# Kernel optimization log

Hardware: AMD Instinct MI355X
Metric: run time of the kernel (lower is better)

Reference implementation:

```python
import jax, jax.numpy as jnp
import numpy as np

EMBED_DIM = 32
HIDDEN_DIM = 64
N = 1024
LN_EPS = 1e-5


def setup_inputs() -> dict:
    key = jax.random.key(0)
    ks = jax.random.split(key, 8)
    d, h = EMBED_DIM, HIDDEN_DIM
    s1 = 1.0 / np.sqrt(2 * d)
    s2 = 1.0 / np.sqrt(h)
    return {
        "node_embeddings": jax.random.normal(ks[0], (N, d), dtype=jnp.float32),
        # Linear(2d -> h), stored as (2d, h) for x @ W
        "W1": jax.random.uniform(ks[1], (2 * d, h), jnp.float32, -s1, s1),
        "b1": jnp.zeros((h,), jnp.float32),
        "g1": jnp.ones((h,), jnp.float32),
        "be1": jnp.zeros((h,), jnp.float32),
        "W2": jax.random.uniform(ks[2], (h, h), jnp.float32, -s2, s2),
        "b2": jnp.zeros((h,), jnp.float32),
        "g2": jnp.ones((h,), jnp.float32),
        "be2": jnp.zeros((h,), jnp.float32),
        "W3": jax.random.uniform(ks[3], (h, 1), jnp.float32, -s2, s2),
        "b3": jnp.zeros((1,), jnp.float32),
    }


def _layernorm(x, gamma, beta):
    mu = jnp.mean(x, axis=-1, keepdims=True)
    var = jnp.mean(jnp.square(x - mu), axis=-1, keepdims=True)
    return (x - mu) * jax.lax.rsqrt(var + LN_EPS) * gamma + beta


def reference(node_embeddings, W1, b1, g1, be1, W2, b2, g2, be2, W3, b3):
    n, d = node_embeddings.shape
    # pair_emb = cat([src_emb, dst_emb], -1); first linear applied without
    # materializing the concat: split W1 into src/dst halves.
    W1s, W1d = W1[:d], W1[d:]
    hs = node_embeddings @ W1s          # (N, h)
    hd = node_embeddings @ W1d          # (N, h)
    h = hs[:, None, :] + hd[None, :, :] + b1   # (N, N, h)
    h = jax.nn.relu(_layernorm(h, g1, be1))
    h = jax.nn.relu(_layernorm(h @ W2 + b2, g2, be2))
    out = jax.nn.sigmoid((h @ W3 + b3)[..., 0])  # (N, N)
    return out
```

## Files before the change

### kernel.cpp

```cpp
#include <hip/hip_runtime.h>
#include <hip/hip_bf16.h>

#define NN 1024
#define ED 32
#define HD 64
#define LN_EPS 1e-5f

typedef short bf16x8 __attribute__((ext_vector_type(8)));
typedef float f32x4 __attribute__((ext_vector_type(4)));

#define OFF_HS   0
#define OFF_HDB  65536
#define OFF_SS   131072
#define OFF_SD   132096
#define OFF_G1   133120
#define OFF_BE1  133184
#define OFF_B2   133248
#define OFF_G2   133312
#define OFF_BE2  133376
#define OFF_W3   133440
#define OFF_B3   133504
#define OFF_SB2  133505
#define OFF_W2F  133508

__device__ __forceinline__ bool buf_is_f32(const void* g1) {
  return *(const unsigned int*)g1 == 0x3F800000u;
}
template <bool F32>
__device__ __forceinline__ float ld(const void* p, int i) {
  return F32 ? ((const float*)p)[i]
             : __bfloat162float(((const __hip_bfloat16*)p)[i]);
}
__device__ __forceinline__ unsigned short f2bf(float f) {
  unsigned int b = __builtin_bit_cast(unsigned int, f);
  b += 0x7FFFu + ((b >> 16) & 1u);
  return (unsigned short)(b >> 16);
}
__device__ __forceinline__ unsigned int pack2bf(float a, float b) {
  return (unsigned int)f2bf(a) | ((unsigned int)f2bf(b) << 16);
}
__device__ __forceinline__ unsigned int pk_bf(float a, float b) {
  __hip_bfloat162 p = __float22bfloat162_rn(make_float2(a, b));
  unsigned int u;
  __builtin_memcpy(&u, &p, 4);
  return u;
}
__device__ __forceinline__ f32x4 splat4(float v) { f32x4 r = {v, v, v, v}; return r; }

template <int CTRL>
__device__ __forceinline__ float dpp_add(float v) {
  int m = __builtin_amdgcn_update_dpp(0, __builtin_bit_cast(int, v), CTRL, 0xF, 0xF, true);
  return v + __builtin_bit_cast(float, m);
}
template <int CTRL>
__device__ __forceinline__ float dpp_mov(float v) {
  return __builtin_bit_cast(float,
      __builtin_amdgcn_update_dpp(0, __builtin_bit_cast(int, v), CTRL, 0xF, 0xF, true));
}
__device__ __forceinline__ float red16(float v) {
  v = dpp_add<0xB1>(v);
  v = dpp_add<0x4E>(v);
  v = dpp_add<0x124>(v);
  v = dpp_add<0x128>(v);
  return v;
}

template <bool F32>
__device__ void prep_body(const void* E, const void* W1, const void* b1,
                          const void* g1, const void* be1, const void* W2,
                          const void* b2, const void* g2, const void* be2,
                          const void* W3, const void* b3, float* ws) {
  const int i = blockIdx.x, t = threadIdx.x;
  if (i < NN) {
    __shared__ float e[ED];
    if (t < ED) e[t] = ld<F32>(E, i * ED + t);
    __syncthreads();
    int k = t & 63;
    bool dside = t >= 64;
    int wofs = dside ? ED * HD : 0;
    float acc = 0.f;
#pragma unroll
    for (int c = 0; c < ED; ++c)
      acc = fmaf(e[c], ld<F32>(W1, wofs + c * HD + k), acc);
    if (dside) acc += ld<F32>(b1, k);
    float s = acc;
#pragma unroll
    for (int m = 1; m <= 32; m <<= 1) s += __shfl_xor(s, m);
    if (dside) {
      ws[OFF_HDB + i * HD + k] = acc;
      if (k == 0) ws[OFF_SD + i] = s;
    } else {
      ws[OFF_HS + i * HD + k] = acc;
      if (k == 0) ws[OFF_SS + i] = s;
    }
  } else if (i < NN + 16) {
    if (t < 32) {
      int d = (i - NN) * 32 + t;
      int lv = d & 63, nt = (d >> 6) & 3, kc = d >> 8;
      int k0 = kc * 32 + ((lv >> 4) & 3) * 8;
      int n = nt * 16 + (lv & 15);
      unsigned int u4[4];
#pragma unroll
      for (int jj = 0; jj < 4; ++jj)
        u4[jj] = pack2bf(ld<F32>(W2, (k0 + 2 * jj) * HD + n),
                         ld<F32>(W2, (k0 + 2 * jj + 1) * HD + n));
      ((uint4*)(ws + OFF_W2F))[d] = make_uint4(u4[0], u4[1], u4[2], u4[3]);
    }
  } else {
    __shared__ float rs[64];
    if (t < 64) {
      ws[OFF_G1  + t] = ld<F32>(g1,  t);
      ws[OFF_BE1 + t] = ld<F32>(be1, t);
      ws[OFF_B2  + t] = ld<F32>(b2,  t);
      ws[OFF_G2  + t] = ld<F32>(g2,  t);
      ws[OFF_BE2 + t] = ld<F32>(be2, t);
      ws[OFF_W3  + t] = ld<F32>(W3,  t);
      float s = 0.f;
      for (int n = 0; n < HD; ++n) s += ld<F32>(W2, t * HD + n);
      rs[t] = s;
    }
    if (t == 64) {
      float s = 0.f;
      for (int n = 0; n < HD; ++n) s += ld<F32>(b2, n);
      ws[OFF_SB2] = s;
    }
    if (t == 65) ws[OFF_B3] = ld<F32>(b3, 0);
    __syncthreads();
    unsigned short* st = (unsigned short*)(ws + OFF_W2F) + 4096;
    for (int s = t; s < 1024; s += 128) {
      int j = s & 7, lv = (s >> 3) & 63, kc = s >> 9;
      st[s] = f2bf(rs[kc * 32 + ((lv >> 4) & 3) * 8 + j]);
    }
  }
}

__global__ __launch_bounds__(128) void prep_kern(
    const void* E, const void* W1, const void* b1, const void* g1,
    const void* be1, const void* W2, const void* b2, const void* g2,
    const void* be2, const void* W3, const void* b3, float* ws) {
  if (buf_is_f32(g1))
    prep_body<true >(E, W1, b1, g1, be1, W2, b2, g2, be2, W3, b3, ws);
  else
    prep_body<false>(E, W1, b1, g1, be1, W2, b2, g2, be2, W3, b3, ws);
}

__global__ __launch_bounds__(256, 4) void pair_kern(
    const float* __restrict__ ws, float* __restrict__ out) {
  __shared__ float sh[1024];
  __shared__ float sdt[1024];
  __shared__ __align__(16) unsigned int X[256 * 32];
  const int t = threadIdx.x;
  const int bid = blockIdx.x;
  const int lid = (bid & 7) * 512 + (bid >> 3);
  const int bi = lid >> 6, bj = lid & 63;
  const int l = t & 63, w = t >> 6;
  const int q = l >> 4, ln = l & 15;
  const int il = t >> 4, jl = t & 15;
  const float inv = 1.f / 64.f;

  {
    int r = t >> 4, c4 = t & 15;
    ((f32x4*)sh )[r * 16 + (c4 ^ r)] = ((const f32x4*)(ws + OFF_HS  + (bi * 16 + r) * HD))[c4];
    ((f32x4*)sdt)[r * 16 + (c4 ^ r)] = ((const f32x4*)(ws + OFF_HDB + (bj * 16 + r) * HD))[c4];
  }
  const float ssum = ws[OFF_SS + bi * 16 + il];
  const float dsum = ws[OFF_SD + bj * 16 + jl];
  __syncthreads();

  const f32x4* A4 = (const f32x4*)sh;
  const f32x4* B4 = (const f32x4*)sdt;

  float r1, nmu;
  {
    f32x4 q4 = splat4(0.f);
#pragma unroll
    for (int c = 0; c < 16; ++c) {
      f32x4 x = A4[il * 16 + (c ^ il)] + B4[jl * 16 + (c ^ jl)];
      q4 = __builtin_elementwise_fma(x, x, q4);
    }
    float ssq = (q4[0] + q4[1]) + (q4[2] + q4[3]);
    float mu = (ssum + dsum) * inv;
    r1 = rsqrtf(fmaf(-mu, mu, ssq * inv) + LN_EPS);
    nmu = -mu * r1;
  }
  asm volatile("" ::: "memory");

  {
    f32x4 r1v = splat4(r1), nm = splat4(nmu), zero = splat4(0.f);
    uint4* Xr4 = (uint4*)(X + t * 32);
#pragma unroll
    for (int b = 0; b < 8; ++b) {
      unsigned int uu[4];
#pragma unroll
      for (int h = 0; h < 2; ++h) {
        int c = 2 * b + h;
        f32x4 x = A4[il * 16 + (c ^ il)] + B4[jl * 16 + (c ^ jl)];
        f32x4 g, be;
#pragma unroll
        for (int e = 0; e < 4; ++e) {
          g[e]  = ws[OFF_G1  + c * 4 + e];
          be[e] = ws[OFF_BE1 + c * 4 + e];
        }
        f32x4 u = __builtin_elementwise_fma(x, r1v, nm);
        f32x4 v = __builtin_elementwise_fma(u, g, be);
        v = __builtin_elementwise_max(v, zero);
        uu[2 * h]     = pk_bf(v[0], v[1]);
        uu[2 * h + 1] = pk_bf(v[2], v[3]);
      }
      Xr4[b ^ (t & 7)] = make_uint4(uu[0], uu[1], uu[2], uu[3]);
    }
  }

  bf16x8 bf[2][4], bsum[2];
  const uint4* WF4 = (const uint4*)(ws + OFF_W2F);
#pragma unroll
  for (int kc = 0; kc < 2; ++kc) {
#pragma unroll
    for (int nt = 0; nt < 4; ++nt)
      bf[kc][nt] = __builtin_bit_cast(bf16x8, WF4[(kc * 4 + nt) * 64 + l]);
    bsum[kc] = __builtin_bit_cast(bf16x8, WF4[512 + kc * 64 + l]);
  }
  float b2v[4], g2v[4], be2v[4], w3v[4];
#pragma unroll
  for (int nt = 0; nt < 4; ++nt) {
    int cix = nt * 16 + ln;
    b2v[nt]  = ws[OFF_B2  + cix];
    g2v[nt]  = ws[OFF_G2  + cix];
    be2v[nt] = ws[OFF_BE2 + cix];
    w3v[nt]  = ws[OFF_W3  + cix];
  }
  const float b3s = ws[OFF_B3];
  const float Sb2 = ws[OFF_SB2];

  const uint4* XL = (const uint4*)X;
  const bool pb0 = (l & 1) != 0, pb1 = (l & 2) != 0;
  const bool pb2 = (l & 4) != 0, pb3 = (l & 8) != 0;
  float zq[4];
#pragma unroll
  for (int mt = 0; mt < 4; ++mt) {
    int m = w * 64 + mt * 16 + ln;
    bf16x8 a0 = __builtin_bit_cast(bf16x8, XL[m * 8 + (q ^ (m & 7))]);
    bf16x8 a1 = __builtin_bit_cast(bf16x8, XL[m * 8 + ((q + 4) ^ (m & 7))]);
    f32x4 acc5[5];
#pragma unroll
    for (int nt = 0; nt < 5; ++nt) {
      bf16x8 b0  = (nt < 4) ? bf[0][nt] : bsum[0];
      bf16x8 b1f = (nt < 4) ? bf[1][nt] : bsum[1];
      f32x4 z4 = splat4(nt < 4 ? b2v[nt] : Sb2);
      z4 = __builtin_amdgcn_mfma_f32_16x16x32_bf16(a0, b0, z4, 0, 0, 0);
      acc5[nt] = __builtin_amdgcn_mfma_f32_16x16x32_bf16(a1, b1f, z4, 0, 0, 0);
    }
    f32x4 qq = splat4(0.f);
#pragma unroll
    for (int nt = 0; nt < 4; ++nt)
      qq = __builtin_elementwise_fma(acc5[nt], acc5[nt], qq);
#pragma unroll
    for (int e = 0; e < 4; ++e) qq[e] = red16(qq[e]);
    f32x4 mu = acc5[4] * splat4(inv);
    f32x4 var = __builtin_elementwise_fma(qq, splat4(inv), -(mu * mu));
    f32x4 r2;
#pragma unroll
    for (int e = 0; e < 4; ++e) r2[e] = rsqrtf(var[e] + LN_EPS);
    f32x4 nm2 = -(mu * r2);
    f32x4 z4 = splat4(0.f);
#pragma unroll
    for (int nt = 0; nt < 4; ++nt) {
      f32x4 u = __builtin_elementwise_fma(acc5[nt], r2, nm2);
      f32x4 v = __builtin_elementwise_fma(u, splat4(g2v[nt]), splat4(be2v[nt]));
      v = __builtin_elementwise_max(v, splat4(0.f));
      z4 = __builtin_elementwise_fma(v, splat4(w3v[nt]), z4);
    }
    float ka0 = pb3 ? z4[2] : z4[0], da0 = pb3 ? z4[0] : z4[2];
    float ka1 = pb3 ? z4[3] : z4[1], da1 = pb3 ? z4[1] : z4[3];
    float za0 = ka0 + dpp_mov<0x128>(da0);
    float za1 = ka1 + dpp_mov<0x128>(da1);
    float kb = pb2 ? za1 : za0, db = pb2 ? za0 : za1;
    zq[mt] = kb + dpp_mov<0x141>(db);
  }

  float kc0 = pb1 ? zq[2] : zq[0], dc0 = pb1 ? zq[0] : zq[2];
  float kc1 = pb1 ? zq[3] : zq[1], dc1 = pb1 ? zq[1] : zq[3];
  float zc0 = kc0 + dpp_mov<0x4E>(dc0);
  float zc1 = kc1 + dpp_mov<0x4E>(dc1);
  float kd = pb0 ? zc1 : zc0, dd = pb0 ? zc0 : zc1;
  float zfin = kd + dpp_mov<0xB1>(dd);

  float o = 1.f / (1.f + __expf(-(zfin + b3s)));
  out[(bi * 16 + w * 4 + (l & 3)) * NN + bj * 16 + q * 4 + ((l >> 2) & 3)] = o;
}

extern "C" void kernel_launch(void* const* d_in, const int* in_sizes, int n_in,
                              void* d_out, int out_size, void* d_ws, size_t ws_size,
                              hipStream_t stream) {
  float* ws = (float*)d_ws;
  hipLaunchKernelGGL(prep_kern, dim3(NN + 17), dim3(128), 0, stream,
                     d_in[0], d_in[1], d_in[2], d_in[3], d_in[4], d_in[5],
                     d_in[6], d_in[7], d_in[8], d_in[9], d_in[10], ws);
  hipLaunchKernelGGL(pair_kern, dim3(4096), dim3(256), 0, stream,
                     ws, (float*)d_out);
}
```

Before: 112.8 us.

## Compute LayerNorm-1 variance from precomputed squares plus an MFMA cross term

The first LayerNorm's sum of squares over (hs+hd) is now expanded as sum(hs^2) + sum(hd^2) + 2*hs·hd. The prep kernel precomputes the per-row squared sums, and the cross dot products for each 16x16 tile come from two bf16 MFMAs instead of a 16-step LDS-read-and-FMA loop per thread. The W2 fragment global loads are also moved earlier so they overlap the LayerNorm-1 work. The cost is precision: the cross term is rounded to bf16 and the variance comes from an E[x^2]-mu^2 form, which can lose accuracy through cancellation.

New measurement: 113.4 us. About the same (+0.5%).

```diff
diff --git a/kernel.cpp b/kernel.cpp
--- a/kernel.cpp
+++ b/kernel.cpp
@@ -22,6 +22,8 @@
 #define OFF_B3   133504
 #define OFF_SB2  133505
 #define OFF_W2F  133508
+#define OFF_SQS  136068
+#define OFF_SQD  137092
 
 __device__ __forceinline__ bool buf_is_f32(const void* g1) {
   return *(const unsigned int*)g1 == 0x3F800000u;
@@ -83,15 +85,18 @@
     for (int c = 0; c < ED; ++c)
       acc = fmaf(e[c], ld<F32>(W1, wofs + c * HD + k), acc);
     if (dside) acc += ld<F32>(b1, k);
-    float s = acc;
-#pragma unroll
-    for (int m = 1; m <= 32; m <<= 1) s += __shfl_xor(s, m);
+    float s = acc, s2 = acc * acc;
+#pragma unroll
+    for (int m = 1; m <= 32; m <<= 1) {
+      s  += __shfl_xor(s,  m);
+      s2 += __shfl_xor(s2, m);
+    }
     if (dside) {
       ws[OFF_HDB + i * HD + k] = acc;
-      if (k == 0) ws[OFF_SD + i] = s;
+      if (k == 0) { ws[OFF_SD + i] = s; ws[OFF_SQD + i] = s2; }
     } else {
       ws[OFF_HS + i * HD + k] = acc;
-      if (k == 0) ws[OFF_SS + i] = s;
+      if (k == 0) { ws[OFF_SS + i] = s; ws[OFF_SQS + i] = s2; }
     }
   } else if (i < NN + 16) {
     if (t < 32) {
@@ -163,8 +168,10 @@
     ((f32x4*)sh )[r * 16 + (c4 ^ r)] = ((const f32x4*)(ws + OFF_HS  + (bi * 16 + r) * HD))[c4];
     ((f32x4*)sdt)[r * 16 + (c4 ^ r)] = ((const f32x4*)(ws + OFF_HDB + (bj * 16 + r) * HD))[c4];
   }
-  const float ssum = ws[OFF_SS + bi * 16 + il];
-  const float dsum = ws[OFF_SD + bj * 16 + jl];
+  const float ssum = ws[OFF_SS  + bi * 16 + il];
+  const float dsum = ws[OFF_SD  + bj * 16 + jl];
+  const float ssqa = ws[OFF_SQS + bi * 16 + il];
+  const float ssqb = ws[OFF_SQD + bj * 16 + jl];
   __syncthreads();
 
   const f32x4* A4 = (const f32x4*)sh;
@@ -172,18 +179,44 @@
 
   float r1, nmu;
   {
-    f32x4 q4 = splat4(0.f);
-#pragma unroll
-    for (int c = 0; c < 16; ++c) {
-      f32x4 x = A4[il * 16 + (c ^ il)] + B4[jl * 16 + (c ^ jl)];
-      q4 = __builtin_elementwise_fma(x, x, q4);
-    }
-    float ssq = (q4[0] + q4[1]) + (q4[2] + q4[3]);
-    float mu = (ssum + dsum) * inv;
-    r1 = rsqrtf(fmaf(-mu, mu, ssq * inv) + LN_EPS);
+    const int rowA = (w << 2) + (ln >> 2);
+    const int q2 = q << 1;
+    f32x4 fa0 = A4[rowA * 16 + ((q2    ) ^ rowA)];
+    f32x4 fa1 = A4[rowA * 16 + ((q2 + 1) ^ rowA)];
+    f32x4 fa2 = A4[rowA * 16 + ((q2 + 8) ^ rowA)];
+    f32x4 fa3 = A4[rowA * 16 + ((q2 + 9) ^ rowA)];
+    f32x4 fb0 = B4[ln * 16 + ((q2    ) ^ ln)];
+    f32x4 fb1 = B4[ln * 16 + ((q2 + 1) ^ ln)];
+    f32x4 fb2 = B4[ln * 16 + ((q2 + 8) ^ ln)];
+    f32x4 fb3 = B4[ln * 16 + ((q2 + 9) ^ ln)];
+    uint4 a0u = make_uint4(pk_bf(fa0[0], fa0[1]), pk_bf(fa0[2], fa0[3]),
+                           pk_bf(fa1[0], fa1[1]), pk_bf(fa1[2], fa1[3]));
+    uint4 a1u = make_uint4(pk_bf(fa2[0], fa2[1]), pk_bf(fa2[2], fa2[3]),
+                           pk_bf(fa3[0], fa3[1]), pk_bf(fa3[2], fa3[3]));
+    uint4 b0u = make_uint4(pk_bf(fb0[0], fb0[1]), pk_bf(fb0[2], fb0[3]),
+                           pk_bf(fb1[0], fb1[1]), pk_bf(fb1[2], fb1[3]));
+    uint4 b1u = make_uint4(pk_bf(fb2[0], fb2[1]), pk_bf(fb2[2], fb2[3]),
+                           pk_bf(fb3[0], fb3[1]), pk_bf(fb3[2], fb3[3]));
+    f32x4 cd = splat4(0.f);
+    cd = __builtin_amdgcn_mfma_f32_16x16x32_bf16(
+        __builtin_bit_cast(bf16x8, a0u), __builtin_bit_cast(bf16x8, b0u), cd, 0, 0, 0);
+    cd = __builtin_amdgcn_mfma_f32_16x16x32_bf16(
+        __builtin_bit_cast(bf16x8, a1u), __builtin_bit_cast(bf16x8, b1u), cd, 0, 0, 0);
+    float mu  = (ssum + dsum) * inv;
+    float ex2 = fmaf(2.f, cd[0], ssqa + ssqb) * inv;
+    r1 = rsqrtf(fmaf(-mu, mu, ex2) + LN_EPS);
     nmu = -mu * r1;
   }
-  asm volatile("" ::: "memory");
+
+  bf16x8 bf[2][4], bsum[2];
+  const uint4* WF4 = (const uint4*)(ws + OFF_W2F);
+#pragma unroll
+  for (int kc = 0; kc < 2; ++kc) {
+#pragma unroll
+    for (int nt = 0; nt < 4; ++nt)
+      bf[kc][nt] = __builtin_bit_cast(bf16x8, WF4[(kc * 4 + nt) * 64 + l]);
+    bsum[kc] = __builtin_bit_cast(bf16x8, WF4[512 + kc * 64 + l]);
+  }
 
   {
     f32x4 r1v = splat4(r1), nm = splat4(nmu), zero = splat4(0.f);
@@ -211,15 +244,6 @@
     }
   }
 
-  bf16x8 bf[2][4], bsum[2];
-  const uint4* WF4 = (const uint4*)(ws + OFF_W2F);
-#pragma unroll
-  for (int kc = 0; kc < 2; ++kc) {
-#pragma unroll
-    for (int nt = 0; nt < 4; ++nt)
-      bf[kc][nt] = __builtin_bit_cast(bf16x8, WF4[(kc * 4 + nt) * 64 + l]);
-    bsum[kc] = __builtin_bit_cast(bf16x8, WF4[512 + kc * 64 + l]);
-  }
   float b2v[4], g2v[4], be2v[4], w3v[4];
 #pragma unroll
   for (int nt = 0; nt < 4; ++nt) {
```
